# Kernel optimization log

Measured on AMD Instinct MI355X. Metric: run time of the kernel, lower is better.

The kernel has to match this reference:

```python
import jax, jax.numpy as jnp
import numpy as np

TEXT_DIM = 1024
FEAT_DIM = 1024
NUM_HEADS = 16
HEAD_DIM = FEAT_DIM // NUM_HEADS
EPS = 1e-6


def rms_norm(x, w):
    # LlamaRMSNorm: compute in fp32, scale by learned weight
    xf = x.astype(jnp.float32)
    var = jnp.mean(xf * xf, axis=-1, keepdims=True)
    return (xf * jax.lax.rsqrt(var + EPS)).astype(x.dtype) * w


def setup_inputs() -> dict:
    key = jax.random.key(0)
    ks = jax.random.split(key, 8)
    def xavier(k, shape, gain=1.0):
        fan_in, fan_out = shape[1], shape[0]
        lim = gain * np.sqrt(6.0 / (fan_in + fan_out))
        return jax.random.uniform(k, shape, jnp.float32, -lim, lim)
    return {
        "text": jax.random.normal(ks[0], (8, 512, TEXT_DIM), jnp.float32),
        "features": jax.random.normal(ks[1], (8, 1024, FEAT_DIM), jnp.float32),
        "W_q": xavier(ks[2], (FEAT_DIM, TEXT_DIM)),
        "b_q": jnp.zeros((FEAT_DIM,), jnp.float32),
        "W_k": xavier(ks[3], (FEAT_DIM, FEAT_DIM)),
        "b_k": jnp.zeros((FEAT_DIM,), jnp.float32),
        "W_o": xavier(ks[4], (FEAT_DIM, FEAT_DIM), gain=0.1),
        "b_o": jnp.zeros((FEAT_DIM,), jnp.float32),
        "g_feat": jnp.ones((FEAT_DIM,), jnp.float32),
        "g_q": jnp.ones((FEAT_DIM,), jnp.float32),
        "g_k": jnp.ones((FEAT_DIM,), jnp.float32),
    }


def reference(text, features, W_q, b_q, W_k, b_k, W_o, b_o, g_feat, g_q, g_k):
    B, T, _ = text.shape
    _, N, _ = features.shape
    feats = rms_norm(features, g_feat)                      # [B,N,Df]
    Q = rms_norm(text @ W_q.T + b_q, g_q)                   # [B,T,Df]
    K = rms_norm(feats @ W_k.T + b_k, g_k)                  # [B,N,Df]
    Qh = Q.reshape(B, T, NUM_HEADS, HEAD_DIM)
    Kh = K.reshape(B, N, NUM_HEADS, HEAD_DIM)
    Vh = feats.reshape(B, N, NUM_HEADS, HEAD_DIM)
    scores = jnp.einsum("bthd,bnhd->bhtn", Qh, Kh) / np.sqrt(HEAD_DIM).astype(np.float32)
    attn = jax.nn.softmax(scores, axis=-1)                  # [B,H,T,N]
    out = jnp.einsum("bhtn,bnhd->bthd", attn, Vh).reshape(B, T, FEAT_DIM)
    return out @ W_o.T + b_o
```

## Files before the change

kernel.cpp:

```cpp
#include <hip/hip_runtime.h>
#include <hip/hip_bf16.h>


typedef unsigned short u16;
typedef __bf16 bf16x8 __attribute__((ext_vector_type(8)));
typedef float f32x4 __attribute__((ext_vector_type(4)));

__device__ inline f32x4 mfma16(bf16x8 a, bf16x8 b, f32x4 c) {
    return __builtin_amdgcn_mfma_f32_16x16x32_bf16(a, b, c, 0, 0, 0);
}

__device__ inline u16 f2bf(float f) {
    union { float f; unsigned u; } v; v.f = f;
    unsigned r = v.u + 0x7fffu + ((v.u >> 16) & 1u);
    return (u16)(r >> 16);
}

__device__ inline float bf2f(u16 x) {
    union { unsigned u; float f; } v; v.u = ((unsigned)x) << 16; return v.f;
}

__device__ inline unsigned pk_bf16(float a, float b) {
    union { float f; unsigned u; } x, y; x.f = a; y.f = b;
    return __builtin_amdgcn_perm(y.u + 0x8000u, x.u + 0x8000u, 0x07060302u);
}

__device__ inline void load_lds16(const void* g, void* l) {
    __builtin_amdgcn_global_load_lds(
        (const __attribute__((address_space(1))) void*)g,
        (__attribute__((address_space(3))) void*)l, 16, 0, 0);
}

__global__ __launch_bounds__(256) void cast_rows_kernel(const float* __restrict__ text,
                                                        const float* __restrict__ Wq,
                                                        const float* __restrict__ Wk,
                                                        const float* __restrict__ Wo,
                                                        const float* __restrict__ features,
                                                        u16* __restrict__ otext, u16* __restrict__ oWq,
                                                        u16* __restrict__ oWk, u16* __restrict__ oWo,
                                                        float* __restrict__ ssbuf) {
    int blk = blockIdx.x, tid = threadIdx.x;
    if (blk < 7168) {
        int i = blk * 256 + tid;
        const float* src; u16* dst; int off;
        if (i < 1048576)      { src = text; dst = otext; off = i; }
        else if (i < 1310720) { src = Wq;   dst = oWq;   off = i - 1048576; }
        else if (i < 1572864) { src = Wk;   dst = oWk;   off = i - 1310720; }
        else                  { src = Wo;   dst = oWo;   off = i - 1572864; }
        float4 v = ((const float4*)src)[off];
        uint2 p; p.x = pk_bf16(v.x, v.y); p.y = pk_bf16(v.z, v.w);
        ((uint2*)dst)[off] = p;
    } else {
        int row = (blk - 7168) * 4 + (tid >> 6);
        int lane = tid & 63;
        const float4* rp = (const float4*)(features + (size_t)row * 1024) + lane * 4;
        float ss = 0.0f;
        #pragma unroll
        for (int i = 0; i < 4; ++i) {
            float4 v = rp[i];
            ss += v.x * v.x + v.y * v.y + v.z * v.z + v.w * v.w;
        }
        #pragma unroll
        for (int m = 1; m < 64; m <<= 1) ss += __shfl_xor(ss, m, 64);
        if (lane == 0) ssbuf[row] = ss;
    }
}

__global__ __launch_bounds__(256) void normT_kernel(const float* __restrict__ features,
                                                    const float* __restrict__ ssbuf,
                                                    const float* __restrict__ g,
                                                    u16* __restrict__ feats_bf,
                                                    u16* __restrict__ Vt) {
    __shared__ __align__(16) u16 tile[64][72];
    int tid = threadIdx.x, b = blockIdx.z;
    int n0 = blockIdx.x * 64, d0 = blockIdx.y * 64;
    int r = tid >> 2, cs = (tid & 3) * 16;
    int grow = b * 1024 + n0 + r;

    float rs = rsqrtf(ssbuf[grow] * (1.0f / 1024.0f) + 1e-6f);
    const float4* src = (const float4*)(features + (size_t)grow * 1024 + d0 + cs);
    const float4* gp  = (const float4*)(g + d0 + cs);
    union { u16 s[16]; uint4 v[2]; } ob;
    #pragma unroll
    for (int i = 0; i < 4; ++i) {
        float4 v = src[i], gv = gp[i];
        unsigned lo = pk_bf16(v.x * rs * gv.x, v.y * rs * gv.y);
        unsigned hi = pk_bf16(v.z * rs * gv.z, v.w * rs * gv.w);
        ((unsigned*)ob.s)[i * 2]     = lo;
        ((unsigned*)ob.s)[i * 2 + 1] = hi;
    }
    uint4* dst = (uint4*)(feats_bf + (size_t)grow * 1024 + d0 + cs);
    dst[0] = ob.v[0]; dst[1] = ob.v[1];
    #pragma unroll
    for (int i = 0; i < 16; ++i) tile[r][cs + i] = ob.s[i];
    __syncthreads();
    union { u16 s[8]; uint4 v; } t0, t1;
    #pragma unroll
    for (int i = 0; i < 8; ++i) { t0.s[i] = tile[cs + i][r]; t1.s[i] = tile[cs + 8 + i][r]; }
    u16* tdst = Vt + ((size_t)(b * 1024 + d0 + r)) * 1024 + n0 + cs;
    *(uint4*)tdst = t0.v;
    *(uint4*)(tdst + 8) = t1.v;
}

__global__ __launch_bounds__(256) void rmsnorm_qk_kernel(u16* __restrict__ QK,
                                                         const float* __restrict__ g_q,
                                                         const float* __restrict__ g_k,
                                                         float qscale) {
    int tid = threadIdx.x;
    int row = blockIdx.x * 4 + (tid >> 6);
    int lane = tid & 63;
    const float* g = (row < 4096) ? g_q : g_k;
    float outsc = (row < 4096) ? qscale : 1.0f;

    u16* rp = QK + (size_t)row * 1024 + lane * 16;
    union { u16 s[16]; uint4 v[2]; } in;
    in.v[0] = *(const uint4*)rp;
    in.v[1] = *(const uint4*)(rp + 8);
    float x[16], ss = 0.0f;
    #pragma unroll
    for (int i = 0; i < 16; ++i) { x[i] = bf2f(in.s[i]); ss += x[i] * x[i]; }
    #pragma unroll
    for (int m = 1; m < 64; m <<= 1) ss += __shfl_xor(ss, m, 64);
    float rs = rsqrtf(ss * (1.0f / 1024.0f) + 1e-6f) * outsc;
    const float4* gp = (const float4*)(g + lane * 16);
    union { unsigned u[8]; uint4 v[2]; } ob;
    #pragma unroll
    for (int i = 0; i < 4; ++i) {
        float4 gv = gp[i];
        ob.u[i * 2]     = pk_bf16(x[i * 4 + 0] * rs * gv.x, x[i * 4 + 1] * rs * gv.y);
        ob.u[i * 2 + 1] = pk_bf16(x[i * 4 + 2] * rs * gv.z, x[i * 4 + 3] * rs * gv.w);
    }
    *(uint4*)rp = ob.v[0];
    *(uint4*)(rp + 8) = ob.v[1];
}

template <bool BF16OUT>
__device__ __forceinline__ void gemm64_bk64(const u16* __restrict__ A, const u16* __restrict__ B,
                                            const float* __restrict__ bias, void* __restrict__ Cout,
                                            int m_blk, int n_blk, int K, int N,
                                            u16* As, u16* Bs) {
    int tid = threadIdx.x, wave = tid >> 6, lane = tid & 63;
    int quad = lane >> 4, l15 = lane & 15;
    int wm = wave & 1, wn = wave >> 1;
    int arow = tid >> 2, ac = (tid & 3) * 8;

    f32x4 acc[4][2] = {};

    for (int k0 = 0; k0 < K; k0 += 64) {
        #pragma unroll
        for (int kh = 0; kh < 2; ++kh)
            #pragma unroll
            for (int rh = 0; rh < 2; ++rh)
                load_lds16(A + (size_t)(m_blk + rh * 64 + arow) * K + k0 + kh * 32 + ac,
                           As + kh * 4096 + rh * 2048 + (wave * 64) * 8);
        #pragma unroll
        for (int kh = 0; kh < 2; ++kh)
            load_lds16(B + (size_t)(n_blk + arow) * K + k0 + kh * 32 + ac,
                       Bs + kh * 2048 + (wave * 64) * 8);
        __syncthreads();
        #pragma unroll
        for (int kh = 0; kh < 2; ++kh) {
            bf16x8 af[4], bfr[2];
            #pragma unroll
            for (int t = 0; t < 4; ++t)
                af[t] = *(const bf16x8*)&As[kh * 4096 + (wm * 64 + t * 16 + l15) * 32 + quad * 8];
            #pragma unroll
            for (int t = 0; t < 2; ++t)
                bfr[t] = *(const bf16x8*)&Bs[kh * 2048 + (wn * 32 + t * 16 + l15) * 32 + quad * 8];
            #pragma unroll
            for (int mt = 0; mt < 4; ++mt)
                #pragma unroll
                for (int nt = 0; nt < 2; ++nt)
                    acc[mt][nt] = mfma16(af[mt], bfr[nt], acc[mt][nt]);
        }
        __syncthreads();
    }
    #pragma unroll
    for (int nt = 0; nt < 2; ++nt) {
        int col = n_blk + wn * 32 + nt * 16 + l15;
        float bv = bias[col];
        #pragma unroll
        for (int mt = 0; mt < 4; ++mt) {
            int row0 = m_blk + wm * 64 + mt * 16 + quad * 4;
            #pragma unroll
            for (int r = 0; r < 4; ++r) {
                float val = acc[mt][nt][r] + bv;
                if (BF16OUT) ((u16*)Cout)[(size_t)(row0 + r) * N + col] = f2bf(val);
                else       ((float*)Cout)[(size_t)(row0 + r) * N + col] = val;
            }
        }
    }
}

__global__ __launch_bounds__(256) void gemm_qk_kernel(const u16* __restrict__ text_bf,
                                                      const u16* __restrict__ Wq,
                                                      const u16* __restrict__ feats_bf,
                                                      const u16* __restrict__ Wk,
                                                      const float* __restrict__ b_q,
                                                      const float* __restrict__ b_k,
                                                      u16* __restrict__ QK) {
    __shared__ __align__(16) u16 As[2 * 128 * 32];
    __shared__ __align__(16) u16 Bs[2 * 64 * 32];
    int id = blockIdx.x;
    if (id < 512) {
        gemm64_bk64<true>(text_bf, Wq, b_q, QK, (id & 31) * 128, (id >> 5) * 64, 1024, 1024, As, Bs);
    } else {
        id -= 512;
        gemm64_bk64<true>(feats_bf, Wk, b_k, QK + 4096 * 1024,
                          (id & 63) * 128, (id >> 6) * 64, 1024, 1024, As, Bs);
    }
}

__global__ __launch_bounds__(256) void gemm_o_kernel(const u16* __restrict__ A,
                                                     const u16* __restrict__ B,
                                                     const float* __restrict__ bias,
                                                     float* __restrict__ C) {
    __shared__ __align__(16) u16 As[2 * 128 * 32];
    __shared__ __align__(16) u16 Bs[2 * 64 * 32];
    int id = blockIdx.x;
    gemm64_bk64<false>(A, B, bias, C, (id & 31) * 128, (id >> 5) * 64, 1024, 1024, As, Bs);
}

__global__ __launch_bounds__(256) void attn_kernel(const u16* __restrict__ Q,
                                                   const u16* __restrict__ K,
                                                   const u16* __restrict__ Vt,
                                                   u16* __restrict__ Out) {
    int bh = blockIdx.x, qt = blockIdx.y;
    int b = bh >> 4, h = bh & 15;
    int tid = threadIdx.x, wave = tid >> 6, lane = tid & 63;
    int quad = lane >> 4, l15 = lane & 15;

    __shared__ __align__(16) u16 Ks[2][64 * 64];
    __shared__ __align__(16) u16 Vs[2][64 * 64];
    __shared__ __align__(16) u16 Plds[4][16 * 64];
    u16* Pw = &Plds[wave][0];
    const int psw = (l15 & 7) << 3;

    const size_t qoff = ((size_t)(b * 512 + qt * 64 + wave * 16 + l15)) * 1024 + h * 64 + quad * 8;
    bf16x8 qf0 = *(const bf16x8*)(Q + qoff);
    bf16x8 qf1 = *(const bf16x8*)(Q + qoff + 32);

    int srl = lane >> 3, scl = lane & 7;
    const u16* Kbase = K + ((size_t)(b * 1024)) * 1024 + h * 64;
    const u16* Vbase = Vt + ((size_t)(b * 1024 + h * 64)) * 1024;

    __bf16 onev = (__bf16)1.0f;
    bf16x8 ones = {onev, onev, onev, onev, onev, onev, onev, onev};

    f32x4 o[4] = {};
    f32x4 lac = {0.0f, 0.0f, 0.0f, 0.0f};

    auto stage = [&](int buf, int n0) {
        #pragma unroll
        for (int j = 0; j < 2; ++j) {
            int row = wave * 16 + j * 8 + srl;
            load_lds16(Kbase + (size_t)(n0 + row) * 1024 + (scl ^ srl) * 8,
                       &Ks[buf][(wave * 16 + j * 8) * 64]);
            load_lds16(Vbase + (size_t)row * 1024 + n0 + (scl ^ srl) * 8,
                       &Vs[buf][(wave * 16 + j * 8) * 64]);
        }
    };

    stage(0, 0);
    __syncthreads();
    int cur = 0;

    for (int n0 = 0; n0 < 1024; n0 += 64) {
        if (n0 < 960) stage(cur ^ 1, n0 + 64);

        f32x4 s[4];
        #pragma unroll
        for (int nt = 0; nt < 4; ++nt) {
            int R = nt * 16 + l15;
            int c1 = (quad ^ (l15 & 7)) * 8;
            bf16x8 kf0 = *(const bf16x8*)&Ks[cur][R * 64 + c1];
            bf16x8 kf1 = *(const bf16x8*)&Ks[cur][R * 64 + (c1 ^ 32)];
            f32x4 z = {-16.0f, -16.0f, -16.0f, -16.0f};
            s[nt] = mfma16(kf0, qf0, z);
            s[nt] = mfma16(kf1, qf1, s[nt]);
        }

        #pragma unroll
        for (int nt = 0; nt < 4; ++nt) {
            uint2 pk;
            pk.x = pk_bf16(exp2f(s[nt][0]), exp2f(s[nt][1]));
            pk.y = pk_bf16(exp2f(s[nt][2]), exp2f(s[nt][3]));
            *(uint2*)&Pw[l15 * 64 + ((nt * 16 + quad * 4) ^ psw)] = pk;
        }

        bf16x8 pf[2];
        #pragma unroll
        for (int kc = 0; kc < 2; ++kc)
            pf[kc] = *(const bf16x8*)&Pw[l15 * 64 + ((kc * 32 + quad * 8) ^ psw)];
        #pragma unroll
        for (int kc = 0; kc < 2; ++kc) {
            lac = mfma16(ones, pf[kc], lac);
            #pragma unroll
            for (int dt = 0; dt < 4; ++dt) {
                int d = dt * 16 + l15;
                int ch = ((kc * 4 + quad) ^ (l15 & 7)) * 8;
                bf16x8 vf = *(const bf16x8*)&Vs[cur][d * 64 + ch];
                o[dt] = mfma16(vf, pf[kc], o[dt]);
            }
        }

        __syncthreads();
        cur ^= 1;
    }

    float il = 1.0f / lac[0];
    size_t obase = ((size_t)(b * 512 + qt * 64 + wave * 16 + l15)) * 1024 + h * 64 + quad * 4;
    #pragma unroll
    for (int dt = 0; dt < 4; ++dt) {
        uint2 pk;
        pk.x = pk_bf16(o[dt][0] * il, o[dt][1] * il);
        pk.y = pk_bf16(o[dt][2] * il, o[dt][3] * il);
        *(uint2*)(Out + obase + dt * 16) = pk;
    }
}

extern "C" void kernel_launch(void* const* d_in, const int* in_sizes, int n_in,
                              void* d_out, int out_size, void* d_ws, size_t ws_size,
                              hipStream_t stream) {
    const float* text     = (const float*)d_in[0];
    const float* features = (const float*)d_in[1];
    const float* W_q      = (const float*)d_in[2];
    const float* b_q      = (const float*)d_in[3];
    const float* W_k      = (const float*)d_in[4];
    const float* b_k      = (const float*)d_in[5];
    const float* W_o      = (const float*)d_in[6];
    const float* b_o      = (const float*)d_in[7];
    const float* g_feat   = (const float*)d_in[8];
    const float* g_q      = (const float*)d_in[9];
    const float* g_k      = (const float*)d_in[10];

    char* ws = (char*)d_ws;
    u16*   text_bf  = (u16*)(ws + 0);
    u16*   Wq_bf    = (u16*)(ws + 8388608);
    u16*   Wk_bf    = (u16*)(ws + 10485760);
    u16*   Wo_bf    = (u16*)(ws + 12582912);
    u16*   feats_bf = (u16*)(ws + 14680064);
    u16*   Vt       = (u16*)(ws + 31457280);
    u16*   QKbuf    = (u16*)(ws + 48234496);
    u16*   attn_bf  = (u16*)(ws + 73400320);
    float* ssbuf    = (float*)(ws + 81788928);

    const float QSCALE = 0.18033688011112042f;

    cast_rows_kernel<<<9216, 256, 0, stream>>>(text, W_q, W_k, W_o, features,
                                               text_bf, Wq_bf, Wk_bf, Wo_bf, ssbuf);
    normT_kernel<<<dim3(16, 16, 8), 256, 0, stream>>>(features, ssbuf, g_feat, feats_bf, Vt);
    gemm_qk_kernel<<<1536, 256, 0, stream>>>(text_bf, Wq_bf, feats_bf, Wk_bf, b_q, b_k, QKbuf);
    rmsnorm_qk_kernel<<<3072, 256, 0, stream>>>(QKbuf, g_q, g_k, QSCALE);
    attn_kernel<<<dim3(128, 8), 256, 0, stream>>>(QKbuf, QKbuf + 4096 * 1024, Vt, attn_bf);
    gemm_o_kernel<<<512, 256, 0, stream>>>(attn_bf, Wo_bf, b_o, (float*)d_out);
}
```

Measured before the change: 227.2 us.

## Double-buffer GEMM LDS tiles with XOR swizzle and add MFMA priority hints

```diff
diff --git a/kernel.cpp b/kernel.cpp
--- a/kernel.cpp
+++ b/kernel.cpp
@@ -142,31 +142,47 @@
     int tid = threadIdx.x, wave = tid >> 6, lane = tid & 63;
     int quad = lane >> 4, l15 = lane & 15;
     int wm = wave & 1, wn = wave >> 1;
-    int arow = tid >> 2, ac = (tid & 3) * 8;
+    int srl = lane >> 3, scl = lane & 7;
+    const int swz = (scl ^ srl) * 8;
 
     f32x4 acc[4][2] = {};
 
+    auto stage = [&](int buf, int k0) {
+        u16* Ad = As + buf * (128 * 64);
+        u16* Bd = Bs + buf * (64 * 64);
+        #pragma unroll
+        for (int is = 0; is < 4; ++is) {
+            int row = is * 32 + wave * 8 + srl;
+            load_lds16(A + (size_t)(m_blk + row) * K + k0 + swz,
+                       Ad + (is * 32 + wave * 8) * 64);
+        }
+        #pragma unroll
+        for (int is = 0; is < 2; ++is) {
+            int row = is * 32 + wave * 8 + srl;
+            load_lds16(B + (size_t)(n_blk + row) * K + k0 + swz,
+                       Bd + (is * 32 + wave * 8) * 64);
+        }
+    };
+
+    stage(0, 0);
+    __syncthreads();
+    int cur = 0;
+
     for (int k0 = 0; k0 < K; k0 += 64) {
-        #pragma unroll
-        for (int kh = 0; kh < 2; ++kh)
-            #pragma unroll
-            for (int rh = 0; rh < 2; ++rh)
-                load_lds16(A + (size_t)(m_blk + rh * 64 + arow) * K + k0 + kh * 32 + ac,
-                           As + kh * 4096 + rh * 2048 + (wave * 64) * 8);
-        #pragma unroll
-        for (int kh = 0; kh < 2; ++kh)
-            load_lds16(B + (size_t)(n_blk + arow) * K + k0 + kh * 32 + ac,
-                       Bs + kh * 2048 + (wave * 64) * 8);
-        __syncthreads();
+        if (k0 + 64 < K) stage(cur ^ 1, k0 + 64);
+
+        const u16* Ar = As + cur * (128 * 64);
+        const u16* Br = Bs + cur * (64 * 64);
         #pragma unroll
         for (int kh = 0; kh < 2; ++kh) {
             bf16x8 af[4], bfr[2];
+            int co = ((kh * 4 + quad) ^ (l15 & 7)) * 8;
             #pragma unroll
             for (int t = 0; t < 4; ++t)
-                af[t] = *(const bf16x8*)&As[kh * 4096 + (wm * 64 + t * 16 + l15) * 32 + quad * 8];
+                af[t] = *(const bf16x8*)&Ar[(wm * 64 + t * 16 + l15) * 64 + co];
             #pragma unroll
             for (int t = 0; t < 2; ++t)
-                bfr[t] = *(const bf16x8*)&Bs[kh * 2048 + (wn * 32 + t * 16 + l15) * 32 + quad * 8];
+                bfr[t] = *(const bf16x8*)&Br[(wn * 32 + t * 16 + l15) * 64 + co];
             #pragma unroll
             for (int mt = 0; mt < 4; ++mt)
                 #pragma unroll
@@ -174,7 +190,9 @@
                     acc[mt][nt] = mfma16(af[mt], bfr[nt], acc[mt][nt]);
         }
         __syncthreads();
-    }
+        cur ^= 1;
+    }
+
     #pragma unroll
     for (int nt = 0; nt < 2; ++nt) {
         int col = n_blk + wn * 32 + nt * 16 + l15;
@@ -199,8 +217,8 @@
                                                       const float* __restrict__ b_q,
                                                       const float* __restrict__ b_k,
                                                       u16* __restrict__ QK) {
-    __shared__ __align__(16) u16 As[2 * 128 * 32];
-    __shared__ __align__(16) u16 Bs[2 * 64 * 32];
+    __shared__ __align__(16) u16 As[2 * 128 * 64];
+    __shared__ __align__(16) u16 Bs[2 * 64 * 64];
     int id = blockIdx.x;
     if (id < 512) {
         gemm64_bk64<true>(text_bf, Wq, b_q, QK, (id & 31) * 128, (id >> 5) * 64, 1024, 1024, As, Bs);
@@ -215,8 +233,8 @@
                                                      const u16* __restrict__ B,
                                                      const float* __restrict__ bias,
                                                      float* __restrict__ C) {
-    __shared__ __align__(16) u16 As[2 * 128 * 32];
-    __shared__ __align__(16) u16 Bs[2 * 64 * 32];
+    __shared__ __align__(16) u16 As[2 * 128 * 64];
+    __shared__ __align__(16) u16 Bs[2 * 64 * 64];
     int id = blockIdx.x;
     gemm64_bk64<false>(A, B, bias, C, (id & 31) * 128, (id >> 5) * 64, 1024, 1024, As, Bs);
 }
@@ -269,6 +287,7 @@
         if (n0 < 960) stage(cur ^ 1, n0 + 64);
 
         f32x4 s[4];
+        __builtin_amdgcn_s_setprio(1);
         #pragma unroll
         for (int nt = 0; nt < 4; ++nt) {
             int R = nt * 16 + l15;
@@ -279,6 +298,7 @@
             s[nt] = mfma16(kf0, qf0, z);
             s[nt] = mfma16(kf1, qf1, s[nt]);
         }
+        __builtin_amdgcn_s_setprio(0);
 
         #pragma unroll
         for (int nt = 0; nt < 4; ++nt) {
@@ -292,6 +312,7 @@
         #pragma unroll
         for (int kc = 0; kc < 2; ++kc)
             pf[kc] = *(const bf16x8*)&Pw[l15 * 64 + ((kc * 32 + quad * 8) ^ psw)];
+        __builtin_amdgcn_s_setprio(1);
         #pragma unroll
         for (int kc = 0; kc < 2; ++kc) {
             lac = mfma16(ones, pf[kc], lac);
@@ -303,6 +324,7 @@
                 o[dt] = mfma16(vf, pf[kc], o[dt]);
             }
         }
+        __builtin_amdgcn_s_setprio(0);
 
         __syncthreads();
         cur ^= 1;
```

Measured after the change: 225.2 us. About the same (-0.9%).
